# Kernel tuning notes

Hardware: AMD Instinct MI355X
Metric: run time of the kernel (lower is better)

## Reference

```python
import jax, jax.numpy as jnp
import numpy as np

T, I, H, O = 16384, 2048, 2048, 1000


def setup_inputs() -> dict:
    key = jax.random.key(0)
    ks = jax.random.split(key, 4)
    lim_r = 1.0 / np.sqrt(H)  # equinox GRUCell uniform init bound
    lim_l = 1.0 / np.sqrt(H)
    return {
        "x": jax.random.normal(ks[0], (T, I), dtype=jnp.float32),
        "weight_ih": jax.random.uniform(ks[1], (3 * H, I), minval=-lim_r, maxval=lim_r, dtype=jnp.float32),
        "weight_hh": jax.random.uniform(ks[2], (3 * H, H), minval=-lim_r, maxval=lim_r, dtype=jnp.float32),
        "bias": jnp.zeros((3 * H,), jnp.float32),
        "bias_n": jnp.zeros((H,), jnp.float32),
        "w_out": jax.random.uniform(ks[3], (O, H), minval=-lim_l, maxval=lim_l, dtype=jnp.float32),
        "b_out": jnp.zeros((O,), jnp.float32),
        "bias_extra": jnp.zeros((O,), jnp.float32),
    }


def reference(x, weight_ih, weight_hh, bias, bias_n, w_out, b_out, bias_extra):
    h_dim = weight_hh.shape[1]
    # input-side gate pre-activations for all timesteps at once: (T, 3H)
    igates = x @ weight_ih.T + bias

    def step(h, ig):
        hg = weight_hh @ h  # (3H,)
        ir, iz, inn = jnp.split(ig, 3)
        hr, hz, hn = jnp.split(hg, 3)
        r = jax.nn.sigmoid(ir + hr)
        z = jax.nn.sigmoid(iz + hz)
        n = jnp.tanh(inn + r * (hn + bias_n))
        return n + z * (h - n), None  # equinox GRUCell update

    h0 = jnp.zeros((h_dim,), x.dtype)
    h_final, _ = jax.lax.scan(step, h0, igates)
    return w_out @ h_final + b_out + bias_extra
```

## Files before the change

### kernel.cpp

```cpp
#include <hip/hip_runtime.h>
#include <hip/hip_bf16.h>

typedef unsigned int u32;
typedef unsigned short u16;
typedef unsigned long long u64;
using half2_t = __attribute__((ext_vector_type(2))) _Float16;
using half8   = __attribute__((ext_vector_type(8))) _Float16;
using f32x4   = __attribute__((ext_vector_type(4))) float;
using u32x4   = __attribute__((ext_vector_type(4))) u32;

#define TT 16384
#define HDIM 2048
#define N3H 6144
#define ODIM 1000

#define WS_WPACK 0ull
#define WS_PROG  25165824ull
#define WS_IG    117440512ull
#define WS_PAIR  318767104ull
#define WS_NEED  318785536ull

#if __has_builtin(__builtin_amdgcn_fdot2)
__device__ __forceinline__ float fdot2u(u32 a, u32 b, float c) {
  return __builtin_amdgcn_fdot2(__builtin_bit_cast(half2_t, a),
                                __builtin_bit_cast(half2_t, b), c, false);
}
#else
__device__ __forceinline__ float fdot2u(u32 a, u32 b, float c) {
  half2_t x = __builtin_bit_cast(half2_t, a), y = __builtin_bit_cast(half2_t, b);
  return c + (float)x[0] * (float)y[0] + (float)x[1] * (float)y[1];
}
#endif

__device__ __forceinline__ u32x4 poll_load16(const u32* p) {
  u32x4 r;
  asm volatile("global_load_dwordx4 %0, %1, off sc0 sc1\n\ts_waitcnt vmcnt(0)"
               : "=&v"(r) : "v"(p));
  return r;
}
__device__ __forceinline__ u32 cload4_cp(const u32* p) {
  u32 r;
  asm volatile("global_load_dword %0, %1, off sc0 sc1\n\ts_waitcnt vmcnt(0)"
               : "=&v"(r) : "v"(p));
  return r;
}
__device__ __forceinline__ void ld3_f16_cp(const _Float16* p0, const _Float16* p1,
                                           const _Float16* p2, float& a, float& b, float& c) {
  u32 ra, rb, rc;
  asm volatile("global_load_ushort %0, %3, off sc0 sc1\n\t"
               "global_load_ushort %1, %4, off sc0 sc1\n\t"
               "global_load_ushort %2, %5, off sc0 sc1\n\t"
               "s_waitcnt vmcnt(0)"
               : "=&v"(ra), "=&v"(rb), "=&v"(rc)
               : "v"(p0), "v"(p1), "v"(p2));
  a = (float)__builtin_bit_cast(_Float16, (u16)ra);
  b = (float)__builtin_bit_cast(_Float16, (u16)rb);
  c = (float)__builtin_bit_cast(_Float16, (u16)rc);
}
__device__ __forceinline__ void st2_cp(_Float16* p, _Float16 v) {
  u32 u = (u32)__builtin_bit_cast(u16, v);
  asm volatile("global_store_short %0, %1, off sc0 sc1" :: "v"(p), "v"(u) : "memory");
}

__global__ void k_zero(u32* p) {
  p[blockIdx.x * 256 + threadIdx.x] = 0u;
}
__global__ void k_zero_n(u32* p, int n) {
  int i = blockIdx.x * 256 + threadIdx.x;
  if (i < n) p[i] = 0u;
}

__global__ __launch_bounds__(256) void k_pack(const float* __restrict__ whh,
                                              u32* __restrict__ outp) {
  u32 idx = blockIdx.x * 256 + threadIdx.x;
  u32 hrow = idx / 3072;
  u32 rem = idx - hrow * 3072;
  u32 c = rem >> 8;
  u32 lane = (rem >> 2) & 63;
  u32 q = rem & 3;
  u32 dl = c * 4 + q;
  u32 g = dl >> 4;
  u32 m = dl & 15;
  u32 kp = lane * 16 + m;
  const float* src = whh + (size_t)(g * 2048 + hrow) * 2048 + 2 * kp;
  half2_t p;
  p[0] = (_Float16)src[0];
  p[1] = (_Float16)src[1];
  outp[idx] = __builtin_bit_cast(u32, p);
}

__device__ __forceinline__ u32 packf16(float a, float b) {
  half2_t p;
  p[0] = (_Float16)a;
  p[1] = (_Float16)b;
  return __builtin_bit_cast(u32, p);
}

__global__ __launch_bounds__(512) void k_fused(const uint4* __restrict__ wpack,
                                               const _Float16* __restrict__ ig,
                                               const float* __restrict__ bias_n,
                                               u32* pair,
                                               const float* __restrict__ X,
                                               const float* __restrict__ Wih,
                                               const float* __restrict__ bias,
                                               u32* prog) {
  __shared__ __align__(16) u32 smem[4096];
  const int tid = threadIdx.x;

  if (blockIdx.x < 128) {
    u32* lds_h = smem;
    const int l = tid & 63, v = tid >> 6;
    const int wg = blockIdx.x;
    const int r0 = wg * 16 + v * 2;
    const int my_row = r0 + (l & 1);

    u32 wdwA[48], wdwB[48];
    {
      const uint4* wpA = wpack + (size_t)r0 * 768 + l;
      const uint4* wpB = wpA + 768;
#pragma unroll
      for (int c = 0; c < 12; ++c) {
        uint4 a = wpA[(size_t)c * 64];
        wdwA[c * 4] = a.x; wdwA[c * 4 + 1] = a.y; wdwA[c * 4 + 2] = a.z; wdwA[c * 4 + 3] = a.w;
      }
#pragma unroll
      for (int c = 0; c < 12; ++c) {
        uint4 b = wpB[(size_t)c * 64];
        wdwB[c * 4] = b.x; wdwB[c * 4 + 1] = b.y; wdwB[c * 4 + 2] = b.z; wdwB[c * 4 + 3] = b.w;
      }
    }
    const float bn = bias_n[my_row];
    float hm = 0.f;
    u32 hreg[16];
#pragma unroll
    for (int m = 0; m < 16; ++m) hreg[m] = 0;

    int ready_blk = 0;
    {
      for (;;) {
        u32 c = cload4_cp(prog);
        if (c >= 48u) break;
        __builtin_amdgcn_s_sleep(8);
      }
      ready_blk = 1;
    }
    float ig0, ig1, ig2;
    ld3_f16_cp(ig + my_row, ig + 2048 + my_row, ig + 4096 + my_row, ig0, ig1, ig2);

    for (int t = 0; t < TT; ++t) {
      float igr = ig0, igz = ig1, ign = ig2;
      float a0 = 0.f, a1 = 0.f, a2 = 0.f, a3 = 0.f, a4 = 0.f, a5 = 0.f;
      float b0 = 0.f, b1 = 0.f, b2 = 0.f, b3 = 0.f, b4 = 0.f, b5 = 0.f;
#pragma unroll
      for (int m = 0; m < 16; m += 2) {
        a0 = fdot2u(wdwA[m],          hreg[m],     a0);
        b0 = fdot2u(wdwA[m + 1],      hreg[m + 1], b0);
        a1 = fdot2u(wdwA[16 + m],     hreg[m],     a1);
        b1 = fdot2u(wdwA[16 + m + 1], hreg[m + 1], b1);
        a2 = fdot2u(wdwA[32 + m],     hreg[m],     a2);
        b2 = fdot2u(wdwA[32 + m + 1], hreg[m + 1], b2);
        a3 = fdot2u(wdwB[m],          hreg[m],     a3);
        b3 = fdot2u(wdwB[m + 1],      hreg[m + 1], b3);
        a4 = fdot2u(wdwB[16 + m],     hreg[m],     a4);
        b4 = fdot2u(wdwB[16 + m + 1], hreg[m + 1], b4);
        a5 = fdot2u(wdwB[32 + m],     hreg[m],     a5);
        b5 = fdot2u(wdwB[32 + m + 1], hreg[m + 1], b5);
      }
      float s0 = a0 + b0, s1 = a1 + b1, s2 = a2 + b2;
      float s3 = a3 + b3, s4 = a4 + b4, s5 = a5 + b5;
#pragma unroll
      for (int off = 1; off < 64; off <<= 1) {
        s0 += __shfl_xor(s0, off, 64);
        s1 += __shfl_xor(s1, off, 64);
        s2 += __shfl_xor(s2, off, 64);
        s3 += __shfl_xor(s3, off, 64);
        s4 += __shfl_xor(s4, off, 64);
        s5 += __shfl_xor(s5, off, 64);
      }
      u32* pdst = pair + (((t + 1) & 1) << 11);
      u32 pk = 0;
      if (l < 2) {
        float sr = l ? s3 : s0, sz = l ? s4 : s1, sn = l ? s5 : s2;
        float r = 1.f / (1.f + __expf(-(igr + sr)));
        float z = 1.f / (1.f + __expf(-(igz + sz)));
        float nx = ign + r * (sn + bn);
        float e = __expf(-2.f * nx);
        float n = (1.f - e) / (1.f + e);
        hm = n + z * (hm - n);
        pk = ((u32)(t + 1) << 16) | (u32)__builtin_bit_cast(u16, (_Float16)hm);
      }
      u32 pk1 = __shfl(pk, 1, 64);
      if (l == 0)
        __hip_atomic_store((u64*)(pdst + r0), (u64)pk | ((u64)pk1 << 32),
                           __ATOMIC_RELAXED, __HIP_MEMORY_SCOPE_AGENT);
      if (t == TT - 1) break;
      {
        int nb = (t + 1) >> 7;
        if (nb >= ready_blk) {
          const u32* pb = prog + nb;
          for (;;) {
            u32 c = cload4_cp(pb);
            if (c >= 48u) break;
            __builtin_amdgcn_s_sleep(8);
          }
          ready_blk = nb + 1;
        }
        const _Float16* igp = ig + (size_t)(t + 1) * N3H;
        ld3_f16_cp(igp + my_row, igp + 2048 + my_row, igp + 4096 + my_row, ig0, ig1, ig2);
      }
      const u32 tgt = (u32)(t + 1) << 16;
      const u32* pp = pdst + 4 * tid;
      __builtin_amdgcn_s_sleep(10);
      u32x4 d;
      for (;;) {
        d = poll_load16(pp);
        u32 bad = ((d[0] ^ tgt) | (d[1] ^ tgt) | (d[2] ^ tgt) | (d[3] ^ tgt)) & 0xFFFF0000u;
        if (!bad) break;
        __builtin_amdgcn_s_sleep(2);
      }
      __syncthreads();
      u32 p0 = (d[0] & 0xFFFFu) | (d[1] << 16);
      u32 p1 = (d[2] & 0xFFFFu) | (d[3] << 16);
      u32* dst = lds_h + 2 * tid + ((tid >> 3) << 2);
      dst[0] = p0;
      dst[1] = p1;
      __syncthreads();
#pragma unroll
      for (int i = 0; i < 4; ++i) {
        uint4 vv = *(const uint4*)(lds_h + l * 20 + i * 4);
        hreg[i * 4] = vv.x; hreg[i * 4 + 1] = vv.y; hreg[i * 4 + 2] = vv.z; hreg[i * 4 + 3] = vv.w;
      }
    }
  } else {
    _Float16* As = (_Float16*)smem;
    _Float16* Bs = (_Float16*)(smem + 2048);
    const int hid = blockIdx.x - 128;
    const int l = tid & 63, w = tid >> 6;
    const int wr = w >> 2, wc = w & 3;
    const int srow = tid >> 2;
    const int scol = (tid & 3) << 3;

    for (int tile = hid; tile < 6144; tile += 128) {
      const int mb = tile / 48, nb = tile - mb * 48;
      const int m0 = mb * 128, n0 = nb * 128;
      f32x4 acc[4][2] = {};

      for (int k0 = 0; k0 < HDIM; k0 += 32) {
        __syncthreads();
        const float* ap = X + (size_t)(m0 + srow) * HDIM + k0 + scol;
        const float* bp = Wih + (size_t)(n0 + srow) * HDIM + k0 + scol;
        float4 aL = *(const float4*)ap, aH = *(const float4*)(ap + 4);
        float4 bL = *(const float4*)bp, bH = *(const float4*)(bp + 4);
        uint4 av4 = make_uint4(packf16(aL.x, aL.y), packf16(aL.z, aL.w),
                               packf16(aH.x, aH.y), packf16(aH.z, aH.w));
        uint4 bv4 = make_uint4(packf16(bL.x, bL.y), packf16(bL.z, bL.w),
                               packf16(bH.x, bH.y), packf16(bH.z, bH.w));
        *(uint4*)(As + srow * 32 + scol) = av4;
        *(uint4*)(Bs + srow * 32 + scol) = bv4;
        __syncthreads();
        half8 av[4], bv[2];
#pragma unroll
        for (int mi = 0; mi < 4; ++mi)
          av[mi] = *(const half8*)(As + (wr * 64 + mi * 16 + (l & 15)) * 32 + (l >> 4) * 8);
#pragma unroll
        for (int ni = 0; ni < 2; ++ni)
          bv[ni] = *(const half8*)(Bs + (wc * 32 + ni * 16 + (l & 15)) * 32 + (l >> 4) * 8);
#pragma unroll
        for (int mi = 0; mi < 4; ++mi)
#pragma unroll
          for (int ni = 0; ni < 2; ++ni)
            acc[mi][ni] = __builtin_amdgcn_mfma_f32_16x16x32_f16(av[mi], bv[ni], acc[mi][ni], 0, 0, 0);
      }
      _Float16* Cout = (_Float16*)ig;
#pragma unroll
      for (int ni = 0; ni < 2; ++ni) {
        int col = n0 + wc * 32 + ni * 16 + (l & 15);
        float bb = bias[col];
#pragma unroll
        for (int mi = 0; mi < 4; ++mi) {
          int rbase = m0 + wr * 64 + mi * 16 + (l >> 4) * 4;
#pragma unroll
          for (int r = 0; r < 4; ++r)
            st2_cp(Cout + (size_t)(rbase + r) * N3H + col,
                   (_Float16)(acc[mi][ni][r] + bb));
        }
      }
      asm volatile("s_waitcnt vmcnt(0)" ::: "memory");
      __syncthreads();
      if (tid == 0)
        __hip_atomic_fetch_add(prog + mb, 1u, __ATOMIC_RELAXED,
                               __HIP_MEMORY_SCOPE_AGENT);
    }
  }
}

__global__ __launch_bounds__(256) void k_out(const float* __restrict__ wout,
                                             const float* __restrict__ bout,
                                             const float* __restrict__ bextra,
                                             const u32* __restrict__ hp,
                                             float* __restrict__ out) {
  const int l = threadIdx.x & 63;
  const int o = blockIdx.x * 4 + (threadIdx.x >> 6);
  if (o >= ODIM) return;
  const float* wr = wout + (size_t)o * HDIM;
  float acc = 0.f;
#pragma unroll
  for (int i = 0; i < 8; ++i) {
    int k4 = i * 256 + l * 4;
    uint4 hd = *(const uint4*)(hp + k4);
    float4 wv = *(const float4*)(wr + k4);
    acc += wv.x * (float)__builtin_bit_cast(_Float16, (u16)(hd.x & 0xFFFFu));
    acc += wv.y * (float)__builtin_bit_cast(_Float16, (u16)(hd.y & 0xFFFFu));
    acc += wv.z * (float)__builtin_bit_cast(_Float16, (u16)(hd.z & 0xFFFFu));
    acc += wv.w * (float)__builtin_bit_cast(_Float16, (u16)(hd.w & 0xFFFFu));
  }
#pragma unroll
  for (int off = 1; off < 64; off <<= 1) acc += __shfl_xor(acc, off, 64);
  if (l == 0) out[o] = acc + bout[o] + bextra[o];
}

__global__ void k_dbg(float* out, float v) {
  int i = blockIdx.x * 256 + threadIdx.x;
  if (i < ODIM) out[i] = v;
}

extern "C" void kernel_launch(void* const* d_in, const int* in_sizes, int n_in,
                              void* d_out, int out_size, void* d_ws, size_t ws_size,
                              hipStream_t stream) {
  const float* x      = (const float*)d_in[0];
  const float* wih    = (const float*)d_in[1];
  const float* whh    = (const float*)d_in[2];
  const float* bias   = (const float*)d_in[3];
  const float* bias_n = (const float*)d_in[4];
  const float* wout   = (const float*)d_in[5];
  const float* bout   = (const float*)d_in[6];
  const float* bextra = (const float*)d_in[7];
  float* out = (float*)d_out;

  if (ws_size < WS_NEED) {
    k_dbg<<<4, 256, 0, stream>>>(out, 1.0e6f + (float)(ws_size / 1048576ull));
    return;
  }

  char* ws = (char*)d_ws;
  u32*      wpack = (u32*)(ws + WS_WPACK);
  u32*      prog  = (u32*)(ws + WS_PROG);
  _Float16* igb   = (_Float16*)(ws + WS_IG);
  u32*      pairb = (u32*)(ws + WS_PAIR);

  k_zero<<<16, 256, 0, stream>>>(pairb);
  k_zero_n<<<1, 256, 0, stream>>>(prog, 128);
  k_pack<<<24576, 256, 0, stream>>>(whh, wpack);

  const uint4* wpc = (const uint4*)wpack;
  const _Float16* igc = igb;
  void* kargs[] = {(void*)&wpc, (void*)&igc, (void*)&bias_n, (void*)&pairb,
                   (void*)&x, (void*)&wih, (void*)&bias, (void*)&prog};
  hipLaunchCooperativeKernel(k_fused, dim3(256), dim3(512), kargs, 0, stream);

  k_out<<<250, 256, 0, stream>>>(wout, bout, bextra, pairb, out);
}
```

Baseline: 34.55 ms.

## Pack hidden-state exchange into 16-bit values with parity-bit epoch flags

Result: slower. 36.39 ms (+5.3%).

```diff
diff --git a/kernel.cpp b/kernel.cpp
--- a/kernel.cpp
+++ b/kernel.cpp
@@ -62,8 +62,9 @@
   asm volatile("global_store_short %0, %1, off sc0 sc1" :: "v"(p), "v"(u) : "memory");
 }
 
-__global__ void k_zero(u32* p) {
-  p[blockIdx.x * 256 + threadIdx.x] = 0u;
+__global__ void k_zero2(u32* p) {
+  int i = blockIdx.x * 256 + threadIdx.x;
+  p[i] = (i >= 1024) ? 0x00010001u : 0u;
 }
 __global__ void k_zero_n(u32* p, int n) {
   int i = blockIdx.x * 256 + threadIdx.x;
@@ -177,8 +178,9 @@
         s4 += __shfl_xor(s4, off, 64);
         s5 += __shfl_xor(s5, off, 64);
       }
-      u32* pdst = pair + (((t + 1) & 1) << 11);
-      u32 pk = 0;
+      u32* pdst = pair + (((t + 1) & 1) << 10);
+      const u32 emask = (((t + 1) >> 1) & 1u) * 0x00010001u;
+      u32 hb = 0;
       if (l < 2) {
         float sr = l ? s3 : s0, sz = l ? s4 : s1, sn = l ? s5 : s2;
         float r = 1.f / (1.f + __expf(-(igr + sr)));
@@ -187,11 +189,11 @@
         float e = __expf(-2.f * nx);
         float n = (1.f - e) / (1.f + e);
         hm = n + z * (hm - n);
-        pk = ((u32)(t + 1) << 16) | (u32)__builtin_bit_cast(u16, (_Float16)hm);
-      }
-      u32 pk1 = __shfl(pk, 1, 64);
+        hb = ((u32)__builtin_bit_cast(u16, (_Float16)hm) + 1u) & 0xFFFEu;
+      }
+      u32 hb1 = __shfl(hb, 1, 64);
       if (l == 0)
-        __hip_atomic_store((u64*)(pdst + r0), (u64)pk | ((u64)pk1 << 32),
+        __hip_atomic_store(pdst + (r0 >> 1), hb | (hb1 << 16) | emask,
                            __ATOMIC_RELAXED, __HIP_MEMORY_SCOPE_AGENT);
       if (t == TT - 1) break;
       {
@@ -208,22 +210,27 @@
         const _Float16* igp = ig + (size_t)(t + 1) * N3H;
         ld3_f16_cp(igp + my_row, igp + 2048 + my_row, igp + 4096 + my_row, ig0, ig1, ig2);
       }
-      const u32 tgt = (u32)(t + 1) << 16;
-      const u32* pp = pdst + 4 * tid;
-      __builtin_amdgcn_s_sleep(10);
       u32x4 d;
-      for (;;) {
-        d = poll_load16(pp);
-        u32 bad = ((d[0] ^ tgt) | (d[1] ^ tgt) | (d[2] ^ tgt) | (d[3] ^ tgt)) & 0xFFFF0000u;
-        if (!bad) break;
-        __builtin_amdgcn_s_sleep(2);
+      d[0] = 0; d[1] = 0; d[2] = 0; d[3] = 0;
+      if (tid < 256) {
+        const u32* pp = pdst + 4 * tid;
+        __builtin_amdgcn_s_sleep(10);
+        for (;;) {
+          d = poll_load16(pp);
+          u32 bad = ((d[0] ^ emask) | (d[1] ^ emask) | (d[2] ^ emask) |
+                     (d[3] ^ emask)) & 0x00010001u;
+          if (!bad) break;
+          __builtin_amdgcn_s_sleep(2);
+        }
       }
       __syncthreads();
-      u32 p0 = (d[0] & 0xFFFFu) | (d[1] << 16);
-      u32 p1 = (d[2] & 0xFFFFu) | (d[3] << 16);
-      u32* dst = lds_h + 2 * tid + ((tid >> 3) << 2);
-      dst[0] = p0;
-      dst[1] = p1;
+      if (tid < 256) {
+        u32* dst = lds_h + 4 * tid + ((tid >> 2) << 2);
+        dst[0] = d[0] & 0xFFFEFFFEu;
+        dst[1] = d[1] & 0xFFFEFFFEu;
+        dst[2] = d[2] & 0xFFFEFFFEu;
+        dst[3] = d[3] & 0xFFFEFFFEu;
+      }
       __syncthreads();
 #pragma unroll
       for (int i = 0; i < 4; ++i) {
@@ -305,14 +312,19 @@
   const float* wr = wout + (size_t)o * HDIM;
   float acc = 0.f;
 #pragma unroll
-  for (int i = 0; i < 8; ++i) {
-    int k4 = i * 256 + l * 4;
-    uint4 hd = *(const uint4*)(hp + k4);
-    float4 wv = *(const float4*)(wr + k4);
-    acc += wv.x * (float)__builtin_bit_cast(_Float16, (u16)(hd.x & 0xFFFFu));
-    acc += wv.y * (float)__builtin_bit_cast(_Float16, (u16)(hd.y & 0xFFFFu));
-    acc += wv.z * (float)__builtin_bit_cast(_Float16, (u16)(hd.z & 0xFFFFu));
-    acc += wv.w * (float)__builtin_bit_cast(_Float16, (u16)(hd.w & 0xFFFFu));
+  for (int i = 0; i < 4; ++i) {
+    int j = i * 256 + l * 4;
+    uint4 hd = *(const uint4*)(hp + j);
+    float4 w0 = *(const float4*)(wr + 2 * j);
+    float4 w1 = *(const float4*)(wr + 2 * j + 4);
+    acc += w0.x * (float)__builtin_bit_cast(_Float16, (u16)(hd.x & 0xFFFEu));
+    acc += w0.y * (float)__builtin_bit_cast(_Float16, (u16)((hd.x >> 16) & 0xFFFEu));
+    acc += w0.z * (float)__builtin_bit_cast(_Float16, (u16)(hd.y & 0xFFFEu));
+    acc += w0.w * (float)__builtin_bit_cast(_Float16, (u16)((hd.y >> 16) & 0xFFFEu));
+    acc += w1.x * (float)__builtin_bit_cast(_Float16, (u16)(hd.z & 0xFFFEu));
+    acc += w1.y * (float)__builtin_bit_cast(_Float16, (u16)((hd.z >> 16) & 0xFFFEu));
+    acc += w1.z * (float)__builtin_bit_cast(_Float16, (u16)(hd.w & 0xFFFEu));
+    acc += w1.w * (float)__builtin_bit_cast(_Float16, (u16)((hd.w >> 16) & 0xFFFEu));
   }
 #pragma unroll
   for (int off = 1; off < 64; off <<= 1) acc += __shfl_xor(acc, off, 64);
@@ -348,7 +360,7 @@
   _Float16* igb   = (_Float16*)(ws + WS_IG);
   u32*      pairb = (u32*)(ws + WS_PAIR);
 
-  k_zero<<<16, 256, 0, stream>>>(pairb);
+  k_zero2<<<8, 256, 0, stream>>>(pairb);
   k_zero_n<<<1, 256, 0, stream>>>(prog, 128);
   k_pack<<<24576, 256, 0, stream>>>(whh, wpack);
 
```
